# Kernel optimization log

Hardware: AMD Instinct MI355X
Metric: run time of the kernel (lower is better)

The kernel has to match this reference:

```python
import jax, jax.numpy as jnp
import numpy as np

N = 50000      # nodes
E = 800000     # edges (avg degree 16)
F_IN = 64      # node_feature_space
H = 64         # hidden_dim
G = 16         # graphs in batch
BN_EPS = 1e-5


def setup_inputs() -> dict:
    key = jax.random.key(0)
    ks = jax.random.split(key, 8)
    x = jax.random.normal(ks[0], (N, F_IN), jnp.float32)
    edge_index = jax.random.randint(ks[1], (2, E), 0, N, dtype=jnp.int64)
    batch = jnp.sort(jax.random.randint(ks[2], (N,), 0, G, dtype=jnp.int64))
    init = lambda k, shp, fan: jax.random.normal(k, shp, jnp.float32) / np.float32(np.sqrt(fan))
    params = dict(
        W1_0=init(ks[3], (F_IN, H), F_IN), b1_0=jnp.zeros((H,), jnp.float32),
        W2_0=init(ks[4], (H, H), H),       b2_0=jnp.zeros((H,), jnp.float32),
        g_0=jnp.ones((H,), jnp.float32),   be_0=jnp.zeros((H,), jnp.float32),
        W1_1=init(ks[5], (H, H), H),       b1_1=jnp.zeros((H,), jnp.float32),
        W2_1=init(ks[6], (H, H), H),       b2_1=jnp.zeros((H,), jnp.float32),
        g_1=jnp.ones((H,), jnp.float32),   be_1=jnp.zeros((H,), jnp.float32),
    )
    return dict(x=x, edge_index=edge_index, batch=batch, **params)


def _gin_layer(x, src, dst, W1, b1, W2, b2, g, be):
    # GINConv (eps=0): h_i = MLP(x_i + sum_{j->i} x_j)
    agg = jax.ops.segment_sum(x[src], dst, num_segments=N)   # [N, d]
    h = x + agg
    h = jnp.maximum(h @ W1 + b1, 0.0) @ W2 + b2              # Linear-ReLU-Linear
    # BatchNorm1d (training-mode batch stats, biased variance as in torch)
    mu = h.mean(axis=0)
    var = h.var(axis=0)
    h = (h - mu) * jax.lax.rsqrt(var + BN_EPS) * g + be
    return jnp.maximum(h, 0.0)                               # ReLU


def reference(x, edge_index, batch,
              W1_0, b1_0, W2_0, b2_0, g_0, be_0,
              W1_1, b1_1, W2_1, b2_1, g_1, be_1):
    src, dst = edge_index[0], edge_index[1]
    x = _gin_layer(x, src, dst, W1_0, b1_0, W2_0, b2_0, g_0, be_0)
    x = _gin_layer(x, src, dst, W1_1, b1_1, W2_1, b2_1, g_1, be_1)
    # global_mean_pool over graph ids
    cnt = jax.ops.segment_sum(jnp.ones((N,), x.dtype), batch, num_segments=G)
    sums = jax.ops.segment_sum(x, batch, num_segments=G)
    h_graph = sums / jnp.maximum(cnt, 1.0)[:, None]
    return (x, h_graph)
```

## Files before the change

### kernel.cpp

```cpp
#include <hip/hip_runtime.h>
#include <hip/hip_bf16.h>


constexpr int NN = 50000;
constexpr int NE = 800000;
constexpr int HD = 64;
constexpr int NG = 16;
constexpr float BN_EPS = 1e-5f;
constexpr int ROWCAP = 64;
constexpr int NPART = 8;
constexpr int PSZ = 6250;
constexpr int PBLK = (PSZ + 3) / 4;

__global__ __launch_bounds__(256)
void prep_kernel(const float* __restrict__ x, __hip_bfloat16* __restrict__ xb,
                 int* __restrict__ cnt, float* __restrict__ stats0,
                 float* __restrict__ stats1, float* __restrict__ psums) {
    int i4 = blockIdx.x * 256 + threadIdx.x;
    if (i4 < NN) cnt[i4] = 0;
    if (blockIdx.x == 0) {
        if (threadIdx.x < 128) stats0[threadIdx.x] = 0.f;
        else stats1[threadIdx.x - 128] = 0.f;
    } else if (blockIdx.x == 1) {
        *(float4*)(psums + threadIdx.x * 4) = make_float4(0.f, 0.f, 0.f, 0.f);
    }
    if (i4 >= NN * HD / 4) return;
    float4 v = *(const float4*)(x + (size_t)i4 * 4);
    union { ushort4 u; __hip_bfloat16 b[4]; } p;
    p.b[0] = __float2bfloat16(v.x);
    p.b[1] = __float2bfloat16(v.y);
    p.b[2] = __float2bfloat16(v.z);
    p.b[3] = __float2bfloat16(v.w);
    *(ushort4*)((unsigned short*)xb + (size_t)i4 * 4) = p.u;
}

__global__ __launch_bounds__(256)
void scatter_kernel(const int* __restrict__ ei, int* __restrict__ cnt,
                    unsigned short* __restrict__ csr) {
    int p = blockIdx.x & 7;
    int chunk = blockIdx.x >> 3;
    int e4 = (chunk * 256 + threadIdx.x) * 4;
    if (e4 >= NE) return;
    int4 s = *(const int4*)(ei + e4);
    int4 d = *(const int4*)(ei + NE + e4);
    int lo = p * PSZ, hi = lo + PSZ;
    int slot;
    if (d.x >= lo && d.x < hi) {
        slot = atomicAdd(&cnt[d.x], 1);
        if (slot < ROWCAP) csr[(d.x << 6) + slot] = (unsigned short)s.x;
    }
    if (d.y >= lo && d.y < hi) {
        slot = atomicAdd(&cnt[d.y], 1);
        if (slot < ROWCAP) csr[(d.y << 6) + slot] = (unsigned short)s.y;
    }
    if (d.z >= lo && d.z < hi) {
        slot = atomicAdd(&cnt[d.z], 1);
        if (slot < ROWCAP) csr[(d.z << 6) + slot] = (unsigned short)s.z;
    }
    if (d.w >= lo && d.w < hi) {
        slot = atomicAdd(&cnt[d.w], 1);
        if (slot < ROWCAP) csr[(d.w << 6) + slot] = (unsigned short)s.w;
    }
}

__global__ __launch_bounds__(256)
void agg_kernel(const float* __restrict__ x, const __hip_bfloat16* __restrict__ xb,
                const int* __restrict__ cnt, const unsigned short* __restrict__ csr,
                float* __restrict__ h) {
    int lr = ((blockIdx.x >> 3) << 2) + (threadIdx.x >> 6);
    if (lr >= PSZ) return;
    int row = (blockIdx.x & 7) * PSZ + lr;
    int lane = threadIdx.x & 63;
    int m = min(cnt[row], ROWCAP);
    int ids = csr[(row << 6) + lane];
    float acc = x[(size_t)row * HD + lane];
    int j = 0;
    float a0 = 0.f, a1 = 0.f, a2 = 0.f, a3 = 0.f;
    float a4 = 0.f, a5 = 0.f, a6 = 0.f, a7 = 0.f;
    for (; j + 8 <= m; j += 8) {
        int nb0 = __shfl(ids, j);
        int nb1 = __shfl(ids, j + 1);
        int nb2 = __shfl(ids, j + 2);
        int nb3 = __shfl(ids, j + 3);
        int nb4 = __shfl(ids, j + 4);
        int nb5 = __shfl(ids, j + 5);
        int nb6 = __shfl(ids, j + 6);
        int nb7 = __shfl(ids, j + 7);
        a0 += __bfloat162float(xb[(size_t)nb0 * HD + lane]);
        a1 += __bfloat162float(xb[(size_t)nb1 * HD + lane]);
        a2 += __bfloat162float(xb[(size_t)nb2 * HD + lane]);
        a3 += __bfloat162float(xb[(size_t)nb3 * HD + lane]);
        a4 += __bfloat162float(xb[(size_t)nb4 * HD + lane]);
        a5 += __bfloat162float(xb[(size_t)nb5 * HD + lane]);
        a6 += __bfloat162float(xb[(size_t)nb6 * HD + lane]);
        a7 += __bfloat162float(xb[(size_t)nb7 * HD + lane]);
    }
    acc += ((a0 + a1) + (a2 + a3)) + ((a4 + a5) + (a6 + a7));
    for (; j < m; j++) {
        int nb = __shfl(ids, j);
        acc += __bfloat162float(xb[(size_t)nb * HD + lane]);
    }
    h[(size_t)row * HD + lane] = acc;
}

__global__ __launch_bounds__(256)
void aggn_kernel(const float* __restrict__ hraw, const __hip_bfloat16* __restrict__ xbr,
                 const int* __restrict__ cnt, const unsigned short* __restrict__ csr,
                 const float* __restrict__ stats_prev, const float* __restrict__ g0,
                 const float* __restrict__ be0, float* __restrict__ h) {
    int lr = ((blockIdx.x >> 3) << 2) + (threadIdx.x >> 6);
    if (lr >= PSZ) return;
    int row = (blockIdx.x & 7) * PSZ + lr;
    int lane = threadIdx.x & 63;
    const float inv = 1.f / (float)NN;
    float mu = stats_prev[lane] * inv;
    float var = stats_prev[64 + lane] * inv - mu * mu;
    float sc = g0[lane] * rsqrtf(var + BN_EPS);
    float off = be0[lane] - mu * sc;
    int m = min(cnt[row], ROWCAP);
    int ids = csr[(row << 6) + lane];
    float acc = fmaxf(fmaf(hraw[(size_t)row * HD + lane], sc, off), 0.f);
    int j = 0;
    float a0 = 0.f, a1 = 0.f, a2 = 0.f, a3 = 0.f;
    float a4 = 0.f, a5 = 0.f, a6 = 0.f, a7 = 0.f;
    for (; j + 8 <= m; j += 8) {
        int nb0 = __shfl(ids, j);
        int nb1 = __shfl(ids, j + 1);
        int nb2 = __shfl(ids, j + 2);
        int nb3 = __shfl(ids, j + 3);
        int nb4 = __shfl(ids, j + 4);
        int nb5 = __shfl(ids, j + 5);
        int nb6 = __shfl(ids, j + 6);
        int nb7 = __shfl(ids, j + 7);
        float v0 = __bfloat162float(xbr[(size_t)nb0 * HD + lane]);
        float v1 = __bfloat162float(xbr[(size_t)nb1 * HD + lane]);
        float v2 = __bfloat162float(xbr[(size_t)nb2 * HD + lane]);
        float v3 = __bfloat162float(xbr[(size_t)nb3 * HD + lane]);
        float v4 = __bfloat162float(xbr[(size_t)nb4 * HD + lane]);
        float v5 = __bfloat162float(xbr[(size_t)nb5 * HD + lane]);
        float v6 = __bfloat162float(xbr[(size_t)nb6 * HD + lane]);
        float v7 = __bfloat162float(xbr[(size_t)nb7 * HD + lane]);
        a0 += fmaxf(fmaf(v0, sc, off), 0.f);
        a1 += fmaxf(fmaf(v1, sc, off), 0.f);
        a2 += fmaxf(fmaf(v2, sc, off), 0.f);
        a3 += fmaxf(fmaf(v3, sc, off), 0.f);
        a4 += fmaxf(fmaf(v4, sc, off), 0.f);
        a5 += fmaxf(fmaf(v5, sc, off), 0.f);
        a6 += fmaxf(fmaf(v6, sc, off), 0.f);
        a7 += fmaxf(fmaf(v7, sc, off), 0.f);
    }
    acc += ((a0 + a1) + (a2 + a3)) + ((a4 + a5) + (a6 + a7));
    for (; j < m; j++) {
        int nb = __shfl(ids, j);
        float v = __bfloat162float(xbr[(size_t)nb * HD + lane]);
        acc += fmaxf(fmaf(v, sc, off), 0.f);
    }
    h[(size_t)row * HD + lane] = acc;
}

__global__ __launch_bounds__(256)
void mlp_kernel(const float* __restrict__ hin, float* __restrict__ hout,
                const float* __restrict__ W1, const float* __restrict__ b1,
                const float* __restrict__ W2, const float* __restrict__ b2,
                float* __restrict__ stats, __hip_bfloat16* __restrict__ xbr) {
    __shared__ float sh[128 * 65];
    __shared__ float sW[64 * 64];
    __shared__ float sb[64];
    __shared__ float red[2][4][64];
    int tid = threadIdx.x;
    int base = blockIdx.x * 128;

    for (int i = tid; i < 4096; i += 256) sW[i] = W1[i];
    if (tid < 64) sb[tid] = b1[tid];
#pragma unroll
    for (int i = 0; i < 8; i++) {
        int i4 = tid + 256 * i;
        int row = i4 >> 4, col = (i4 & 15) * 4;
        int grow = base + row;
        float4 v = (grow < NN) ? *(const float4*)(hin + (size_t)grow * HD + col)
                               : make_float4(0.f, 0.f, 0.f, 0.f);
        float* d = sh + row * 65 + col;
        d[0] = v.x; d[1] = v.y; d[2] = v.z; d[3] = v.w;
    }
    __syncthreads();

    int wv = tid >> 6;
    int lane = tid & 63;

    float acc0[16], acc1[16];
#pragma unroll
    for (int j = 0; j < 16; j++) { acc0[j] = sb[wv * 16 + j]; acc1[j] = acc0[j]; }
    for (int k = 0; k < 64; k++) {
        float a0 = sh[lane * 65 + k];
        float a1 = sh[(64 + lane) * 65 + k];
        const float4* wr = (const float4*)(sW + k * 64 + wv * 16);
#pragma unroll
        for (int q = 0; q < 4; q++) {
            float4 w = wr[q];
            acc0[4 * q + 0] = fmaf(a0, w.x, acc0[4 * q + 0]);
            acc0[4 * q + 1] = fmaf(a0, w.y, acc0[4 * q + 1]);
            acc0[4 * q + 2] = fmaf(a0, w.z, acc0[4 * q + 2]);
            acc0[4 * q + 3] = fmaf(a0, w.w, acc0[4 * q + 3]);
            acc1[4 * q + 0] = fmaf(a1, w.x, acc1[4 * q + 0]);
            acc1[4 * q + 1] = fmaf(a1, w.y, acc1[4 * q + 1]);
            acc1[4 * q + 2] = fmaf(a1, w.z, acc1[4 * q + 2]);
            acc1[4 * q + 3] = fmaf(a1, w.w, acc1[4 * q + 3]);
        }
    }
    __syncthreads();

#pragma unroll
    for (int j = 0; j < 16; j++) {
        sh[lane * 65 + wv * 16 + j] = fmaxf(acc0[j], 0.f);
        sh[(64 + lane) * 65 + wv * 16 + j] = fmaxf(acc1[j], 0.f);
    }
    for (int i = tid; i < 4096; i += 256) sW[i] = W2[i];
    if (tid < 64) sb[tid] = b2[tid];
    __syncthreads();

#pragma unroll
    for (int j = 0; j < 16; j++) { acc0[j] = sb[wv * 16 + j]; acc1[j] = acc0[j]; }
    for (int k = 0; k < 64; k++) {
        float a0 = sh[lane * 65 + k];
        float a1 = sh[(64 + lane) * 65 + k];
        const float4* wr = (const float4*)(sW + k * 64 + wv * 16);
#pragma unroll
        for (int q = 0; q < 4; q++) {
            float4 w = wr[q];
            acc0[4 * q + 0] = fmaf(a0, w.x, acc0[4 * q + 0]);
            acc0[4 * q + 1] = fmaf(a0, w.y, acc0[4 * q + 1]);
            acc0[4 * q + 2] = fmaf(a0, w.z, acc0[4 * q + 2]);
            acc0[4 * q + 3] = fmaf(a0, w.w, acc0[4 * q + 3]);
            acc1[4 * q + 0] = fmaf(a1, w.x, acc1[4 * q + 0]);
            acc1[4 * q + 1] = fmaf(a1, w.y, acc1[4 * q + 1]);
            acc1[4 * q + 2] = fmaf(a1, w.z, acc1[4 * q + 2]);
            acc1[4 * q + 3] = fmaf(a1, w.w, acc1[4 * q + 3]);
        }
    }
    __syncthreads();
#pragma unroll
    for (int j = 0; j < 16; j++) {
        sh[lane * 65 + wv * 16 + j] = acc0[j];
        sh[(64 + lane) * 65 + wv * 16 + j] = acc1[j];
    }
    __syncthreads();

#pragma unroll
    for (int i = 0; i < 8; i++) {
        int i4 = tid + 256 * i;
        int row = i4 >> 4, col = (i4 & 15) * 4;
        int grow = base + row;
        if (grow < NN) {
            const float* s = sh + row * 65 + col;
            float4 v = make_float4(s[0], s[1], s[2], s[3]);
            *(float4*)(hout + (size_t)grow * HD + col) = v;
            if (xbr) {
                union { ushort4 u; __hip_bfloat16 b[4]; } p;
                p.b[0] = __float2bfloat16(v.x);
                p.b[1] = __float2bfloat16(v.y);
                p.b[2] = __float2bfloat16(v.z);
                p.b[3] = __float2bfloat16(v.w);
                *(ushort4*)((unsigned short*)xbr + (size_t)grow * HD + col) = p.u;
            }
        }
    }

    {
        int col = tid & 63;
        int r0 = (tid >> 6) * 32;
        float s = 0.f, ss = 0.f;
#pragma unroll
        for (int r = 0; r < 32; r++) {
            float v = (base + r0 + r < NN) ? sh[(r0 + r) * 65 + col] : 0.f;
            s += v;
            ss += v * v;
        }
        red[0][tid >> 6][col] = s;
        red[1][tid >> 6][col] = ss;
        __syncthreads();
        if (tid < 64) {
            float S = red[0][0][col] + red[0][1][col] + red[0][2][col] + red[0][3][col];
            atomicAdd(stats + col, S);
        } else if (tid < 128) {
            float SS = red[1][0][col] + red[1][1][col] + red[1][2][col] + red[1][3][col];
            atomicAdd(stats + 64 + col, SS);
        }
    }
}

__global__ __launch_bounds__(256)
void norm_kernel(float* h, const float* __restrict__ stats,
                 const float* __restrict__ g, const float* __restrict__ be,
                 const int* __restrict__ batch, float* __restrict__ psums) {
    __shared__ float sg[2][64];
    if (threadIdx.x < 128) sg[threadIdx.x >> 6][threadIdx.x & 63] = 0.f;
    __syncthreads();
    size_t i4 = (size_t)blockIdx.x * 256 + threadIdx.x;
    int row = (int)(i4 >> 4);
    int base_row = blockIdx.x * 16;
    int g0 = batch[base_row];
    size_t off = i4 * 4;
    int col = (int)(off & 63);
    float4 v = *(const float4*)(h + off);
    float4 sm = *(const float4*)(stats + col);
    float4 sq = *(const float4*)(stats + 64 + col);
    float4 gg = *(const float4*)(g + col);
    float4 bb = *(const float4*)(be + col);
    const float inv = 1.f / (float)NN;
    float4 o;
    {
        float mu = sm.x * inv, var = sq.x * inv - mu * mu;
        float sc = gg.x * rsqrtf(var + BN_EPS);
        o.x = fmaxf((v.x - mu) * sc + bb.x, 0.f);
    }
    {
        float mu = sm.y * inv, var = sq.y * inv - mu * mu;
        float sc = gg.y * rsqrtf(var + BN_EPS);
        o.y = fmaxf((v.y - mu) * sc + bb.y, 0.f);
    }
    {
        float mu = sm.z * inv, var = sq.z * inv - mu * mu;
        float sc = gg.z * rsqrtf(var + BN_EPS);
        o.z = fmaxf((v.z - mu) * sc + bb.z, 0.f);
    }
    {
        float mu = sm.w * inv, var = sq.w * inv - mu * mu;
        float sc = gg.w * rsqrtf(var + BN_EPS);
        o.w = fmaxf((v.w - mu) * sc + bb.w, 0.f);
    }
    *(float4*)(h + off) = o;

    int dg = batch[row] - g0;
    if (dg <= 1) {
        atomicAdd(&sg[dg][col + 0], o.x);
        atomicAdd(&sg[dg][col + 1], o.y);
        atomicAdd(&sg[dg][col + 2], o.z);
        atomicAdd(&sg[dg][col + 3], o.w);
    } else {
        int gid = g0 + dg;
        atomicAdd(&psums[gid * HD + col + 0], o.x);
        atomicAdd(&psums[gid * HD + col + 1], o.y);
        atomicAdd(&psums[gid * HD + col + 2], o.z);
        atomicAdd(&psums[gid * HD + col + 3], o.w);
    }
    __syncthreads();
    if (threadIdx.x < 128) {
        int d = threadIdx.x >> 6;
        int c = threadIdx.x & 63;
        float s = sg[d][c];
        if (g0 + d < NG && s != 0.f) atomicAdd(&psums[(g0 + d) * HD + c], s);
    }
}

__device__ __forceinline__ int lower_bound_batch(const int* __restrict__ b, int val) {
    int lo = 0, hi = NN;
    while (lo < hi) {
        int mid = (lo + hi) >> 1;
        if (b[mid] < val) lo = mid + 1;
        else hi = mid;
    }
    return lo;
}

__global__ __launch_bounds__(1024)
void pool_finalize_kernel(const float* __restrict__ sums, const int* __restrict__ batch,
                          float* __restrict__ out) {
    int g = threadIdx.x >> 6;
    int col = threadIdx.x & 63;
    int s = lower_bound_batch(batch, g);
    int e = lower_bound_batch(batch, g + 1);
    float cnt = (float)(e - s);
    out[g * HD + col] = sums[g * HD + col] / fmaxf(cnt, 1.f);
}

extern "C" void kernel_launch(void* const* d_in, const int* in_sizes, int n_in,
                              void* d_out, int out_size, void* d_ws, size_t ws_size,
                              hipStream_t stream) {
    const float* x = (const float*)d_in[0];
    const int* ei = (const int*)d_in[1];
    const int* batch = (const int*)d_in[2];
    const float* W1_0 = (const float*)d_in[3];
    const float* b1_0 = (const float*)d_in[4];
    const float* W2_0 = (const float*)d_in[5];
    const float* b2_0 = (const float*)d_in[6];
    const float* g_0 = (const float*)d_in[7];
    const float* be_0 = (const float*)d_in[8];
    const float* W1_1 = (const float*)d_in[9];
    const float* b1_1 = (const float*)d_in[10];
    const float* W2_1 = (const float*)d_in[11];
    const float* b2_1 = (const float*)d_in[12];
    const float* g_1 = (const float*)d_in[13];
    const float* be_1 = (const float*)d_in[14];

    float* out = (float*)d_out;

    float* buf_h = (float*)d_ws;
    float* stats0 = buf_h + (size_t)NN * HD;
    float* stats1 = stats0 + 128;
    float* psums = stats1 + 128;
    int* cnt = (int*)(psums + 1024);
    unsigned short* csr = (unsigned short*)(cnt + NN);
    __hip_bfloat16* xb = (__hip_bfloat16*)(csr + (size_t)NN * ROWCAP);

    dim3 b256(256);
    int mlp_grid = (NN + 127) / 128;
    int norm_grid = (NN * HD / 4 + 255) / 256;
    int sct_grid = ((NE + 1023) / 1024) * NPART;
    int agg_grid = NPART * PBLK;

    prep_kernel<<<norm_grid, b256, 0, stream>>>(x, xb, cnt, stats0, stats1, psums);
    scatter_kernel<<<sct_grid, b256, 0, stream>>>(ei, cnt, csr);

    agg_kernel<<<agg_grid, b256, 0, stream>>>(x, xb, cnt, csr, buf_h);
    mlp_kernel<<<mlp_grid, b256, 0, stream>>>(buf_h, out, W1_0, b1_0, W2_0, b2_0,
                                              stats0, xb);

    aggn_kernel<<<agg_grid, b256, 0, stream>>>(out, xb, cnt, csr,
                                               stats0, g_0, be_0, buf_h);
    mlp_kernel<<<mlp_grid, b256, 0, stream>>>(buf_h, out, W1_1, b1_1, W2_1, b2_1,
                                              stats1, (__hip_bfloat16*)nullptr);

    norm_kernel<<<norm_grid, b256, 0, stream>>>(out, stats1, g_1, be_1, batch, psums);
    pool_finalize_kernel<<<1, dim3(1024), 0, stream>>>(psums, batch, out + (size_t)NN * HD);
}
```

Measured before the change: 275.9 us.

## Fuse neighbor aggregation into the MLP kernel per GIN layer

Merges the separate aggregation and MLP kernels into one templated layer kernel of 512 threads. Each wave gathers 16 rows' neighbor sums straight into shared memory, so the fp32 intermediate buffer is no longer written to and read back from global memory, and two launches disappear. Neighbor ids are broadcast with readlane instead of shuffles. Layer 0's bf16 output goes to a second buffer so other blocks can still gather the original features safely. In exchange, the partition-ordered row mapping that improved cache locality is dropped. Fewer resident blocks and serialized per-wave gathers could also hide latency less well.

```diff
diff --git a/kernel.cpp b/kernel.cpp
--- a/kernel.cpp
+++ b/kernel.cpp
@@ -10,7 +10,10 @@
 constexpr int ROWCAP = 64;
 constexpr int NPART = 8;
 constexpr int PSZ = 6250;
-constexpr int PBLK = (PSZ + 3) / 4;
+
+__device__ __forceinline__ int rdl(int v, int l) {
+    return __builtin_amdgcn_readlane(v, l);
+}
 
 __global__ __launch_bounds__(256)
 void prep_kernel(const float* __restrict__ x, __hip_bfloat16* __restrict__ xb,
@@ -63,191 +66,150 @@
     }
 }
 
-__global__ __launch_bounds__(256)
-void agg_kernel(const float* __restrict__ x, const __hip_bfloat16* __restrict__ xb,
-                const int* __restrict__ cnt, const unsigned short* __restrict__ csr,
-                float* __restrict__ h) {
-    int lr = ((blockIdx.x >> 3) << 2) + (threadIdx.x >> 6);
-    if (lr >= PSZ) return;
-    int row = (blockIdx.x & 7) * PSZ + lr;
-    int lane = threadIdx.x & 63;
-    int m = min(cnt[row], ROWCAP);
-    int ids = csr[(row << 6) + lane];
-    float acc = x[(size_t)row * HD + lane];
-    int j = 0;
-    float a0 = 0.f, a1 = 0.f, a2 = 0.f, a3 = 0.f;
-    float a4 = 0.f, a5 = 0.f, a6 = 0.f, a7 = 0.f;
-    for (; j + 8 <= m; j += 8) {
-        int nb0 = __shfl(ids, j);
-        int nb1 = __shfl(ids, j + 1);
-        int nb2 = __shfl(ids, j + 2);
-        int nb3 = __shfl(ids, j + 3);
-        int nb4 = __shfl(ids, j + 4);
-        int nb5 = __shfl(ids, j + 5);
-        int nb6 = __shfl(ids, j + 6);
-        int nb7 = __shfl(ids, j + 7);
-        a0 += __bfloat162float(xb[(size_t)nb0 * HD + lane]);
-        a1 += __bfloat162float(xb[(size_t)nb1 * HD + lane]);
-        a2 += __bfloat162float(xb[(size_t)nb2 * HD + lane]);
-        a3 += __bfloat162float(xb[(size_t)nb3 * HD + lane]);
-        a4 += __bfloat162float(xb[(size_t)nb4 * HD + lane]);
-        a5 += __bfloat162float(xb[(size_t)nb5 * HD + lane]);
-        a6 += __bfloat162float(xb[(size_t)nb6 * HD + lane]);
-        a7 += __bfloat162float(xb[(size_t)nb7 * HD + lane]);
-    }
-    acc += ((a0 + a1) + (a2 + a3)) + ((a4 + a5) + (a6 + a7));
-    for (; j < m; j++) {
-        int nb = __shfl(ids, j);
-        acc += __bfloat162float(xb[(size_t)nb * HD + lane]);
-    }
-    h[(size_t)row * HD + lane] = acc;
-}
-
-__global__ __launch_bounds__(256)
-void aggn_kernel(const float* __restrict__ hraw, const __hip_bfloat16* __restrict__ xbr,
-                 const int* __restrict__ cnt, const unsigned short* __restrict__ csr,
-                 const float* __restrict__ stats_prev, const float* __restrict__ g0,
-                 const float* __restrict__ be0, float* __restrict__ h) {
-    int lr = ((blockIdx.x >> 3) << 2) + (threadIdx.x >> 6);
-    if (lr >= PSZ) return;
-    int row = (blockIdx.x & 7) * PSZ + lr;
-    int lane = threadIdx.x & 63;
-    const float inv = 1.f / (float)NN;
-    float mu = stats_prev[lane] * inv;
-    float var = stats_prev[64 + lane] * inv - mu * mu;
-    float sc = g0[lane] * rsqrtf(var + BN_EPS);
-    float off = be0[lane] - mu * sc;
-    int m = min(cnt[row], ROWCAP);
-    int ids = csr[(row << 6) + lane];
-    float acc = fmaxf(fmaf(hraw[(size_t)row * HD + lane], sc, off), 0.f);
-    int j = 0;
-    float a0 = 0.f, a1 = 0.f, a2 = 0.f, a3 = 0.f;
-    float a4 = 0.f, a5 = 0.f, a6 = 0.f, a7 = 0.f;
-    for (; j + 8 <= m; j += 8) {
-        int nb0 = __shfl(ids, j);
-        int nb1 = __shfl(ids, j + 1);
-        int nb2 = __shfl(ids, j + 2);
-        int nb3 = __shfl(ids, j + 3);
-        int nb4 = __shfl(ids, j + 4);
-        int nb5 = __shfl(ids, j + 5);
-        int nb6 = __shfl(ids, j + 6);
-        int nb7 = __shfl(ids, j + 7);
-        float v0 = __bfloat162float(xbr[(size_t)nb0 * HD + lane]);
-        float v1 = __bfloat162float(xbr[(size_t)nb1 * HD + lane]);
-        float v2 = __bfloat162float(xbr[(size_t)nb2 * HD + lane]);
-        float v3 = __bfloat162float(xbr[(size_t)nb3 * HD + lane]);
-        float v4 = __bfloat162float(xbr[(size_t)nb4 * HD + lane]);
-        float v5 = __bfloat162float(xbr[(size_t)nb5 * HD + lane]);
-        float v6 = __bfloat162float(xbr[(size_t)nb6 * HD + lane]);
-        float v7 = __bfloat162float(xbr[(size_t)nb7 * HD + lane]);
-        a0 += fmaxf(fmaf(v0, sc, off), 0.f);
-        a1 += fmaxf(fmaf(v1, sc, off), 0.f);
-        a2 += fmaxf(fmaf(v2, sc, off), 0.f);
-        a3 += fmaxf(fmaf(v3, sc, off), 0.f);
-        a4 += fmaxf(fmaf(v4, sc, off), 0.f);
-        a5 += fmaxf(fmaf(v5, sc, off), 0.f);
-        a6 += fmaxf(fmaf(v6, sc, off), 0.f);
-        a7 += fmaxf(fmaf(v7, sc, off), 0.f);
-    }
-    acc += ((a0 + a1) + (a2 + a3)) + ((a4 + a5) + (a6 + a7));
-    for (; j < m; j++) {
-        int nb = __shfl(ids, j);
-        float v = __bfloat162float(xbr[(size_t)nb * HD + lane]);
-        acc += fmaxf(fmaf(v, sc, off), 0.f);
-    }
-    h[(size_t)row * HD + lane] = acc;
-}
-
-__global__ __launch_bounds__(256)
-void mlp_kernel(const float* __restrict__ hin, float* __restrict__ hout,
-                const float* __restrict__ W1, const float* __restrict__ b1,
-                const float* __restrict__ W2, const float* __restrict__ b2,
-                float* __restrict__ stats, __hip_bfloat16* __restrict__ xbr) {
+template <int MODE>
+__global__ __launch_bounds__(512)
+void layer_kernel(const float* __restrict__ xin, const __hip_bfloat16* __restrict__ xg,
+                  const int* __restrict__ cnt, const unsigned short* __restrict__ csr,
+                  const float* __restrict__ stats_prev, const float* __restrict__ gp,
+                  const float* __restrict__ bep,
+                  const float* __restrict__ W1, const float* __restrict__ b1,
+                  const float* __restrict__ W2, const float* __restrict__ b2,
+                  float* __restrict__ hout, float* __restrict__ stats,
+                  __hip_bfloat16* __restrict__ xbr) {
     __shared__ float sh[128 * 65];
     __shared__ float sW[64 * 64];
     __shared__ float sb[64];
-    __shared__ float red[2][4][64];
+    __shared__ float red[2][8][64];
     int tid = threadIdx.x;
     int base = blockIdx.x * 128;
-
-    for (int i = tid; i < 4096; i += 256) sW[i] = W1[i];
+    int w = tid >> 6, lane = tid & 63;
+
+    for (int i = tid; i < 4096; i += 512) sW[i] = W1[i];
     if (tid < 64) sb[tid] = b1[tid];
-#pragma unroll
-    for (int i = 0; i < 8; i++) {
-        int i4 = tid + 256 * i;
-        int row = i4 >> 4, col = (i4 & 15) * 4;
-        int grow = base + row;
-        float4 v = (grow < NN) ? *(const float4*)(hin + (size_t)grow * HD + col)
-                               : make_float4(0.f, 0.f, 0.f, 0.f);
-        float* d = sh + row * 65 + col;
-        d[0] = v.x; d[1] = v.y; d[2] = v.z; d[3] = v.w;
-    }
-    __syncthreads();
-
-    int wv = tid >> 6;
-    int lane = tid & 63;
-
-    float acc0[16], acc1[16];
-#pragma unroll
-    for (int j = 0; j < 16; j++) { acc0[j] = sb[wv * 16 + j]; acc1[j] = acc0[j]; }
+
+    float sc = 1.f, off = 0.f;
+    if (MODE == 1) {
+        const float inv = 1.f / (float)NN;
+        float mu = stats_prev[lane] * inv;
+        float var = stats_prev[64 + lane] * inv - mu * mu;
+        sc = gp[lane] * rsqrtf(var + BN_EPS);
+        off = bep[lane] - mu * sc;
+    }
+
+    for (int rl = w * 16; rl < w * 16 + 16; rl++) {
+        int grow = base + rl;
+        float acc = 0.f;
+        if (grow < NN) {
+            int m = min(cnt[grow], ROWCAP);
+            int ids = (int)csr[((size_t)grow << 6) + lane];
+            float sv = xin[(size_t)grow * HD + lane];
+            acc = (MODE == 1) ? fmaxf(fmaf(sv, sc, off), 0.f) : sv;
+            int j = 0;
+            float a0 = 0.f, a1 = 0.f, a2 = 0.f, a3 = 0.f;
+            float a4 = 0.f, a5 = 0.f, a6 = 0.f, a7 = 0.f;
+            for (; j + 8 <= m; j += 8) {
+                int n0 = rdl(ids, j);
+                int n1 = rdl(ids, j + 1);
+                int n2 = rdl(ids, j + 2);
+                int n3 = rdl(ids, j + 3);
+                int n4 = rdl(ids, j + 4);
+                int n5 = rdl(ids, j + 5);
+                int n6 = rdl(ids, j + 6);
+                int n7 = rdl(ids, j + 7);
+                float v0 = __bfloat162float(xg[((size_t)n0 << 6) + lane]);
+                float v1 = __bfloat162float(xg[((size_t)n1 << 6) + lane]);
+                float v2 = __bfloat162float(xg[((size_t)n2 << 6) + lane]);
+                float v3 = __bfloat162float(xg[((size_t)n3 << 6) + lane]);
+                float v4 = __bfloat162float(xg[((size_t)n4 << 6) + lane]);
+                float v5 = __bfloat162float(xg[((size_t)n5 << 6) + lane]);
+                float v6 = __bfloat162float(xg[((size_t)n6 << 6) + lane]);
+                float v7 = __bfloat162float(xg[((size_t)n7 << 6) + lane]);
+                if (MODE == 1) {
+                    a0 += fmaxf(fmaf(v0, sc, off), 0.f);
+                    a1 += fmaxf(fmaf(v1, sc, off), 0.f);
+                    a2 += fmaxf(fmaf(v2, sc, off), 0.f);
+                    a3 += fmaxf(fmaf(v3, sc, off), 0.f);
+                    a4 += fmaxf(fmaf(v4, sc, off), 0.f);
+                    a5 += fmaxf(fmaf(v5, sc, off), 0.f);
+                    a6 += fmaxf(fmaf(v6, sc, off), 0.f);
+                    a7 += fmaxf(fmaf(v7, sc, off), 0.f);
+                } else {
+                    a0 += v0; a1 += v1; a2 += v2; a3 += v3;
+                    a4 += v4; a5 += v5; a6 += v6; a7 += v7;
+                }
+            }
+            acc += ((a0 + a1) + (a2 + a3)) + ((a4 + a5) + (a6 + a7));
+            for (; j < m; j++) {
+                int nb = rdl(ids, j);
+                float v = __bfloat162float(xg[((size_t)nb << 6) + lane]);
+                acc += (MODE == 1) ? fmaxf(fmaf(v, sc, off), 0.f) : v;
+            }
+        }
+        sh[rl * 65 + lane] = acc;
+    }
+    __syncthreads();
+
+    float acc0[8], acc1[8];
+#pragma unroll
+    for (int j = 0; j < 8; j++) { acc0[j] = sb[w * 8 + j]; acc1[j] = acc0[j]; }
     for (int k = 0; k < 64; k++) {
         float a0 = sh[lane * 65 + k];
         float a1 = sh[(64 + lane) * 65 + k];
-        const float4* wr = (const float4*)(sW + k * 64 + wv * 16);
-#pragma unroll
-        for (int q = 0; q < 4; q++) {
-            float4 w = wr[q];
-            acc0[4 * q + 0] = fmaf(a0, w.x, acc0[4 * q + 0]);
-            acc0[4 * q + 1] = fmaf(a0, w.y, acc0[4 * q + 1]);
-            acc0[4 * q + 2] = fmaf(a0, w.z, acc0[4 * q + 2]);
-            acc0[4 * q + 3] = fmaf(a0, w.w, acc0[4 * q + 3]);
-            acc1[4 * q + 0] = fmaf(a1, w.x, acc1[4 * q + 0]);
-            acc1[4 * q + 1] = fmaf(a1, w.y, acc1[4 * q + 1]);
-            acc1[4 * q + 2] = fmaf(a1, w.z, acc1[4 * q + 2]);
-            acc1[4 * q + 3] = fmaf(a1, w.w, acc1[4 * q + 3]);
-        }
-    }
-    __syncthreads();
-
-#pragma unroll
-    for (int j = 0; j < 16; j++) {
-        sh[lane * 65 + wv * 16 + j] = fmaxf(acc0[j], 0.f);
-        sh[(64 + lane) * 65 + wv * 16 + j] = fmaxf(acc1[j], 0.f);
-    }
-    for (int i = tid; i < 4096; i += 256) sW[i] = W2[i];
+        const float4* wr = (const float4*)(sW + k * 64 + w * 8);
+#pragma unroll
+        for (int q = 0; q < 2; q++) {
+            float4 wv = wr[q];
+            acc0[4 * q + 0] = fmaf(a0, wv.x, acc0[4 * q + 0]);
+            acc0[4 * q + 1] = fmaf(a0, wv.y, acc0[4 * q + 1]);
+            acc0[4 * q + 2] = fmaf(a0, wv.z, acc0[4 * q + 2]);
+            acc0[4 * q + 3] = fmaf(a0, wv.w, acc0[4 * q + 3]);
+            acc1[4 * q + 0] = fmaf(a1, wv.x, acc1[4 * q + 0]);
+            acc1[4 * q + 1] = fmaf(a1, wv.y, acc1[4 * q + 1]);
+            acc1[4 * q + 2] = fmaf(a1, wv.z, acc1[4 * q + 2]);
+            acc1[4 * q + 3] = fmaf(a1, wv.w, acc1[4 * q + 3]);
+        }
+    }
+    __syncthreads();
+
+#pragma unroll
+    for (int j = 0; j < 8; j++) {
+        sh[lane * 65 + w * 8 + j] = fmaxf(acc0[j], 0.f);
+        sh[(64 + lane) * 65 + w * 8 + j] = fmaxf(acc1[j], 0.f);
+    }
+    for (int i = tid; i < 4096; i += 512) sW[i] = W2[i];
     if (tid < 64) sb[tid] = b2[tid];
     __syncthreads();
 
 #pragma unroll
-    for (int j = 0; j < 16; j++) { acc0[j] = sb[wv * 16 + j]; acc1[j] = acc0[j]; }
+    for (int j = 0; j < 8; j++) { acc0[j] = sb[w * 8 + j]; acc1[j] = acc0[j]; }
     for (int k = 0; k < 64; k++) {
         float a0 = sh[lane * 65 + k];
         float a1 = sh[(64 + lane) * 65 + k];
-        const float4* wr = (const float4*)(sW + k * 64 + wv * 16);
-#pragma unroll
-        for (int q = 0; q < 4; q++) {
-            float4 w = wr[q];
-            acc0[4 * q + 0] = fmaf(a0, w.x, acc0[4 * q + 0]);
-            acc0[4 * q + 1] = fmaf(a0, w.y, acc0[4 * q + 1]);
-            acc0[4 * q + 2] = fmaf(a0, w.z, acc0[4 * q + 2]);
-            acc0[4 * q + 3] = fmaf(a0, w.w, acc0[4 * q + 3]);
-            acc1[4 * q + 0] = fmaf(a1, w.x, acc1[4 * q + 0]);
-            acc1[4 * q + 1] = fmaf(a1, w.y, acc1[4 * q + 1]);
-            acc1[4 * q + 2] = fmaf(a1, w.z, acc1[4 * q + 2]);
-            acc1[4 * q + 3] = fmaf(a1, w.w, acc1[4 * q + 3]);
-        }
-    }
-    __syncthreads();
-#pragma unroll
-    for (int j = 0; j < 16; j++) {
-        sh[lane * 65 + wv * 16 + j] = acc0[j];
-        sh[(64 + lane) * 65 + wv * 16 + j] = acc1[j];
-    }
-    __syncthreads();
-
-#pragma unroll
-    for (int i = 0; i < 8; i++) {
-        int i4 = tid + 256 * i;
+        const float4* wr = (const float4*)(sW + k * 64 + w * 8);
+#pragma unroll
+        for (int q = 0; q < 2; q++) {
+            float4 wv = wr[q];
+            acc0[4 * q + 0] = fmaf(a0, wv.x, acc0[4 * q + 0]);
+            acc0[4 * q + 1] = fmaf(a0, wv.y, acc0[4 * q + 1]);
+            acc0[4 * q + 2] = fmaf(a0, wv.z, acc0[4 * q + 2]);
+            acc0[4 * q + 3] = fmaf(a0, wv.w, acc0[4 * q + 3]);
+            acc1[4 * q + 0] = fmaf(a1, wv.x, acc1[4 * q + 0]);
+            acc1[4 * q + 1] = fmaf(a1, wv.y, acc1[4 * q + 1]);
+            acc1[4 * q + 2] = fmaf(a1, wv.z, acc1[4 * q + 2]);
+            acc1[4 * q + 3] = fmaf(a1, wv.w, acc1[4 * q + 3]);
+        }
+    }
+    __syncthreads();
+#pragma unroll
+    for (int j = 0; j < 8; j++) {
+        sh[lane * 65 + w * 8 + j] = acc0[j];
+        sh[(64 + lane) * 65 + w * 8 + j] = acc1[j];
+    }
+    __syncthreads();
+
+#pragma unroll
+    for (int i = 0; i < 4; i++) {
+        int i4 = tid + 512 * i;
         int row = i4 >> 4, col = (i4 & 15) * 4;
         int grow = base + row;
         if (grow < NN) {
@@ -266,24 +228,28 @@
     }
 
     {
-        int col = tid & 63;
-        int r0 = (tid >> 6) * 32;
         float s = 0.f, ss = 0.f;
 #pragma unroll
-        for (int r = 0; r < 32; r++) {
-            float v = (base + r0 + r < NN) ? sh[(r0 + r) * 65 + col] : 0.f;
+        for (int r = 0; r < 16; r++) {
+            int rl = w * 16 + r;
+            float v = (base + rl < NN) ? sh[rl * 65 + lane] : 0.f;
             s += v;
             ss += v * v;
         }
-        red[0][tid >> 6][col] = s;
-        red[1][tid >> 6][col] = ss;
+        red[0][w][lane] = s;
+        red[1][w][lane] = ss;
         __syncthreads();
         if (tid < 64) {
-            float S = red[0][0][col] + red[0][1][col] + red[0][2][col] + red[0][3][col];
-            atomicAdd(stats + col, S);
+            float S = 0.f;
+#pragma unroll
+            for (int q = 0; q < 8; q++) S += red[0][q][tid];
+            atomicAdd(stats + tid, S);
         } else if (tid < 128) {
-            float SS = red[1][0][col] + red[1][1][col] + red[1][2][col] + red[1][3][col];
-            atomicAdd(stats + 64 + col, SS);
+            int c = tid - 64;
+            float SS = 0.f;
+#pragma unroll
+            for (int q = 0; q < 8; q++) SS += red[1][q][c];
+            atomicAdd(stats + 64 + c, SS);
         }
     }
 }
@@ -394,31 +360,30 @@
 
     float* out = (float*)d_out;
 
-    float* buf_h = (float*)d_ws;
-    float* stats0 = buf_h + (size_t)NN * HD;
+    float* stats0 = (float*)d_ws;
     float* stats1 = stats0 + 128;
     float* psums = stats1 + 128;
     int* cnt = (int*)(psums + 1024);
     unsigned short* csr = (unsigned short*)(cnt + NN);
     __hip_bfloat16* xb = (__hip_bfloat16*)(csr + (size_t)NN * ROWCAP);
+    __hip_bfloat16* xb2 = xb + (size_t)NN * HD;
 
     dim3 b256(256);
-    int mlp_grid = (NN + 127) / 128;
+    dim3 b512(512);
+    int layer_grid = (NN + 127) / 128;
     int norm_grid = (NN * HD / 4 + 255) / 256;
     int sct_grid = ((NE + 1023) / 1024) * NPART;
-    int agg_grid = NPART * PBLK;
 
     prep_kernel<<<norm_grid, b256, 0, stream>>>(x, xb, cnt, stats0, stats1, psums);
     scatter_kernel<<<sct_grid, b256, 0, stream>>>(ei, cnt, csr);
 
-    agg_kernel<<<agg_grid, b256, 0, stream>>>(x, xb, cnt, csr, buf_h);
-    mlp_kernel<<<mlp_grid, b256, 0, stream>>>(buf_h, out, W1_0, b1_0, W2_0, b2_0,
-                                              stats0, xb);
-
-    aggn_kernel<<<agg_grid, b256, 0, stream>>>(out, xb, cnt, csr,
-                                               stats0, g_0, be_0, buf_h);
-    mlp_kernel<<<mlp_grid, b256, 0, stream>>>(buf_h, out, W1_1, b1_1, W2_1, b2_1,
-                                              stats1, (__hip_bfloat16*)nullptr);
+    layer_kernel<0><<<layer_grid, b512, 0, stream>>>(
+        x, xb, cnt, csr, nullptr, nullptr, nullptr,
+        W1_0, b1_0, W2_0, b2_0, out, stats0, xb2);
+
+    layer_kernel<1><<<layer_grid, b512, 0, stream>>>(
+        out, xb2, cnt, csr, stats0, g_0, be_0,
+        W1_1, b1_1, W2_1, b2_1, out, stats1, (__hip_bfloat16*)nullptr);
 
     norm_kernel<<<norm_grid, b256, 0, stream>>>(out, stats1, g_1, be_1, batch, psums);
     pool_finalize_kernel<<<1, dim3(1024), 0, stream>>>(psums, batch, out + (size_t)NN * HD);
```

After: 285.1 us. 1.03x slower.
